# Optimization experiments

Hardware: AMD Instinct MI355X
Metric: run time of the kernel (lower is better)

Reference implementation:

```python
import jax, jax.numpy as jnp
import numpy as np

T, B, C = 2048, 8, 1024
H, K, P = 16, 31, 15  # num_heads, kernel_size, padding_l
R = C // H


def setup_inputs() -> dict:
    key = jax.random.key(0)
    k1, k2 = jax.random.split(key)
    x = jax.random.normal(k1, (T, B, C), dtype=jnp.float32)
    # weight_linear.weight, xavier-ish scale, shape (H*K, C)
    W = jax.random.normal(k2, (H * K, C), dtype=jnp.float32) * (2.0 / (C + H * K)) ** 0.5
    return {"x": x, "W": W}


def reference(x, W):
    # per-position dynamic kernels: (T,B,H,K)
    w = jnp.einsum('tbc,oc->tbo', x, W).reshape(T, B, H, K)
    w = jax.nn.softmax(w, axis=-1)  # weight_softmax=True
    # depthwise dynamic conv: out[t] = sum_k w[t,:,:,k] * x[t - P + k]
    xr = x.reshape(T, B, H, R)
    xp = jnp.pad(xr, ((P, K - 1 - P), (0, 0), (0, 0), (0, 0)))
    out = jnp.zeros_like(xr)
    for k in range(K):  # fixed small kernel-size loop, fuses under jit
        out = out + w[:, :, :, k:k + 1] * jax.lax.dynamic_slice_in_dim(xp, k, T, axis=0)
    return out.reshape(T, B, C)
```

## Files before the change

kernel.cpp:

```cpp
#include <hip/hip_runtime.h>
#include <cstddef>
#include <cstdint>

constexpr int T_ = 2048;
constexpr int B_ = 8;
constexpr int C_ = 1024;
constexpr int H_ = 16;
constexpr int K_ = 31;
constexpr int P_ = 15;
constexpr int M_ = T_ * B_;
constexpr int N_ = H_ * K_;
constexpr int NP = 512;

typedef _Float16 f16x4 __attribute__((ext_vector_type(4)));
typedef _Float16 f16x8 __attribute__((ext_vector_type(8)));
typedef float f32x4 __attribute__((ext_vector_type(4)));

__device__ __forceinline__ void async_cp16(const void* g, void* l) {
    __builtin_amdgcn_global_load_lds(
        (const __attribute__((address_space(1))) void*)g,
        (__attribute__((address_space(3))) void*)l, 16, 0, 0);
}

constexpr int XCH = M_ * C_ / 8;
constexpr int WCH = NP * C_ / 8;

__global__ __launch_bounds__(256)
void cvt_inputs(const float* __restrict__ X, const float* __restrict__ W,
                _Float16* __restrict__ Xh, _Float16* __restrict__ Wh) {
    const int id = blockIdx.x * 256 + threadIdx.x;
    if (id < XCH) {
        const float4 v0 = *(const float4*)(X + (size_t)id * 8);
        const float4 v1 = *(const float4*)(X + (size_t)id * 8 + 4);
        f16x8 hv;
        hv[0] = (_Float16)v0.x; hv[1] = (_Float16)v0.y;
        hv[2] = (_Float16)v0.z; hv[3] = (_Float16)v0.w;
        hv[4] = (_Float16)v1.x; hv[5] = (_Float16)v1.y;
        hv[6] = (_Float16)v1.z; hv[7] = (_Float16)v1.w;
        *(f16x8*)(Xh + (size_t)id * 8) = hv;
    } else {
        const int j = id - XCH;
        const int n = j >> 7, sp = j & 127;
        const int h = n >> 5, k = n & 31;
        f16x8 hv = {};
        if (k < 31) {
            const float* wp = W + (size_t)(h * 31 + k) * C_ + sp * 8;
            const float4 v0 = *(const float4*)(wp);
            const float4 v1 = *(const float4*)(wp + 4);
            hv[0] = (_Float16)v0.x; hv[1] = (_Float16)v0.y;
            hv[2] = (_Float16)v0.z; hv[3] = (_Float16)v0.w;
            hv[4] = (_Float16)v1.x; hv[5] = (_Float16)v1.y;
            hv[6] = (_Float16)v1.z; hv[7] = (_Float16)v1.w;
        }
        *(f16x8*)(Wh + (size_t)n * C_ + sp * 8) = hv;
    }
}

__global__ __launch_bounds__(256)
void fused_gsc(const _Float16* __restrict__ Xh, const _Float16* __restrict__ Wh,
               float* __restrict__ out) {
    __shared__ __align__(16) char smem[81920];
    _Float16* const As = (_Float16*)smem;
    _Float16* const Bs = (_Float16*)(smem + 49152);
    _Float16* const Ls = (_Float16*)smem;
    _Float16* const Wls = (_Float16*)(smem + 49152);
    float (* const xs)[64] = (float(*)[64])smem;

    const int tid = threadIdx.x;
    const int lane = tid & 63;
    const int w = tid >> 6;
    const int wm = (w >> 1) * 64;
    const int wn = (w & 1) * 64;
    const int col = lane & 15;
    const int g = lane >> 4;
    const int m0 = blockIdx.x * 128;
    const int n0 = blockIdx.y * 128;

    const _Float16* asrc[4];
    const _Float16* bsrc[4];
#pragma unroll
    for (int p = 0; p < 4; ++p) {
        const int ci = p * 256 + tid;
        const int r = ci >> 3, cs = ci & 7;
        const int cl = cs ^ (r & 7);
        asrc[p] = Xh + (size_t)(m0 + r) * C_ + cl * 8;
        bsrc[p] = Wh + (size_t)(n0 + r) * C_ + cl * 8;
    }

    f32x4 acc[4][4] = {};

#pragma unroll
    for (int p = 0; p < 4; ++p) {
        const int ci = p * 256 + tid;
        async_cp16(asrc[p], As + ci * 8);
    }
#pragma unroll
    for (int p = 0; p < 4; ++p) {
        const int ci = p * 256 + tid;
        async_cp16(bsrc[p], Bs + ci * 8);
    }
#pragma unroll
    for (int p = 0; p < 4; ++p) {
        const int ci = p * 256 + tid;
        async_cp16(asrc[p] + 64, As + 8192 + ci * 8);
    }
    asm volatile("s_waitcnt vmcnt(4)" ::: "memory");
    __builtin_amdgcn_s_barrier();
    __builtin_amdgcn_sched_barrier(0);

    for (int t = 0; t < 16; ++t) {
        const int ca = t % 3, cb = t & 1;
        if (t < 15) {
            const int k1 = (t + 1) * 64;
#pragma unroll
            for (int p = 0; p < 4; ++p) {
                const int ci = p * 256 + tid;
                async_cp16(bsrc[p] + k1, Bs + (cb ^ 1) * 8192 + ci * 8);
            }
        }
        if (t < 14) {
            const int k2 = (t + 2) * 64;
            const int ca2 = (t + 2) % 3;
#pragma unroll
            for (int p = 0; p < 4; ++p) {
                const int ci = p * 256 + tid;
                async_cp16(asrc[p] + k2, As + ca2 * 8192 + ci * 8);
            }
        }

        f16x8 a[2][4], b[2][4];
#pragma unroll
        for (int kk = 0; kk < 2; ++kk) {
#pragma unroll
            for (int mf = 0; mf < 4; ++mf) {
                const int row = wm + mf * 16 + col;
                const int c = ((kk << 2) | g) ^ (row & 7);
                a[kk][mf] = *(const f16x8*)&As[ca * 8192 + row * 64 + c * 8];
            }
#pragma unroll
            for (int nf = 0; nf < 4; ++nf) {
                const int row = wn + nf * 16 + col;
                const int c = ((kk << 2) | g) ^ (row & 7);
                b[kk][nf] = *(const f16x8*)&Bs[cb * 8192 + row * 64 + c * 8];
            }
        }
#pragma unroll
        for (int kk = 0; kk < 2; ++kk)
#pragma unroll
            for (int nf = 0; nf < 4; ++nf)
#pragma unroll
                for (int mf = 0; mf < 4; ++mf)
                    acc[mf][nf] = __builtin_amdgcn_mfma_f32_16x16x32_f16(
                        a[kk][mf], b[kk][nf], acc[mf][nf], 0, 0, 0);

        if (t < 14) {
            asm volatile("s_waitcnt vmcnt(4)" ::: "memory");
        } else {
            asm volatile("s_waitcnt vmcnt(0)" ::: "memory");
        }
        __builtin_amdgcn_s_barrier();
        __builtin_amdgcn_sched_barrier(0);
    }

    const int rb = g * 4;
#pragma unroll
    for (int nf = 0; nf < 4; ++nf) {
        const int nl = wn + nf * 16 + col;
#pragma unroll
        for (int mf = 0; mf < 4; ++mf) {
            const int row = wm + mf * 16 + rb;
#pragma unroll
            for (int r = 0; r < 4; ++r)
                Ls[(row + r) * 136 + nl] = (_Float16)acc[mf][nf][r];
        }
    }
    __syncthreads();

#pragma unroll
    for (int p = 0; p < 2; ++p) {
        const int task = tid + p * 256;
        const int row = task >> 2, hl = task & 3;
        const _Float16* lp = &Ls[row * 136 + hl * 32];
        float v[32];
#pragma unroll
        for (int c = 0; c < 4; ++c) {
            const f16x8 ch = *(const f16x8*)(lp + c * 8);
#pragma unroll
            for (int e = 0; e < 8; ++e) v[c * 8 + e] = (float)ch[e];
        }
        float mx = v[0];
#pragma unroll
        for (int k = 1; k < 31; ++k) mx = fmaxf(mx, v[k]);
        float ssum = 0.f;
#pragma unroll
        for (int k = 0; k < 31; ++k) { v[k] = __expf(v[k] - mx); ssum += v[k]; }
        const float inv = 1.f / ssum;
        _Float16* op = &Wls[(hl * 128 + row) * 32];
#pragma unroll
        for (int c = 0; c < 4; ++c) {
            f16x8 ov;
#pragma unroll
            for (int e = 0; e < 8; ++e) {
                const int k = c * 8 + e;
                ov[e] = (k < 31) ? (_Float16)(v[k] * inv) : (_Float16)0.f;
            }
            *(f16x8*)(op + c * 8) = ov;
        }
    }

    const int t0 = blockIdx.x * 16;
    const int hbase = blockIdx.y * 4;
    const int s = tid & 15;
    const int grp = tid >> 4;
    const int bl = grp & 3;
    const int tquad = (grp >> 2) * 4;

    for (int iter = 0; iter < 8; ++iter) {
        const int hl = iter >> 1, bh = iter & 1;
        const int h = hbase + hl;
        __syncthreads();

        for (int task = tid; task < 184 * 8; task += 256) {
            const int r184 = task >> 3, hc = task & 7;
            const int r46 = r184 >> 2, bb = r184 & 3;
            const int t = t0 + r46 - 15;
            f16x8 v = {};
            if (t >= 0 && t < T_)
                v = *(const f16x8*)(Xh + (size_t)(t * 8 + bh * 4 + bb) * C_ +
                                    h * 64 + hc * 8);
            f32x4 lo, hi;
            lo[0] = (float)v[0]; lo[1] = (float)v[1];
            lo[2] = (float)v[2]; lo[3] = (float)v[3];
            hi[0] = (float)v[4]; hi[1] = (float)v[5];
            hi[2] = (float)v[6]; hi[3] = (float)v[7];
            const int sw = r184 & 7;
            *(f32x4*)&xs[r184][((2 * hc) ^ sw) * 4] = lo;
            *(f32x4*)&xs[r184][((2 * hc + 1) ^ sw) * 4] = hi;
        }
        __syncthreads();

        const int bglob = bh * 4 + bl;
        f32x4 cacc[4] = {};
        f32x4 wc[4];
#pragma unroll
        for (int rr = 0; rr < 34; ++rr) {
            const int r184 = (tquad + rr) * 4 + bl;
            const f32x4 xv = *(const f32x4*)&xs[r184][(s ^ (r184 & 7)) * 4];
#pragma unroll
            for (int i = 0; i < 4; ++i) {
                const int k = rr - i;
                if (k < 0 || k > 30) continue;
                if ((k & 3) == 0) {
                    const f16x4 wq = *(const f16x4*)
                        &Wls[(hl * 128 + (tquad + i) * 8 + bglob) * 32 + k];
                    wc[i][0] = (float)wq[0]; wc[i][1] = (float)wq[1];
                    wc[i][2] = (float)wq[2]; wc[i][3] = (float)wq[3];
                }
                cacc[i] += wc[i][k & 3] * xv;
            }
        }
#pragma unroll
        for (int i = 0; i < 4; ++i) {
            const int t = t0 + tquad + i;
            *(f32x4*)(out + (size_t)(t * 8 + bglob) * C_ + h * 64 + s * 4) =
                cacc[i];
        }
    }
}

extern "C" void kernel_launch(void* const* d_in, const int* in_sizes, int n_in,
                              void* d_out, int out_size, void* d_ws,
                              size_t ws_size, hipStream_t stream) {
    const float* X = (const float*)d_in[0];
    const float* W = (const float*)d_in[1];
    float* out = (float*)d_out;

    _Float16* Wh = (_Float16*)d_ws;
    _Float16* Xh = (_Float16*)((char*)d_ws + (size_t)NP * C_ * 2);

    cvt_inputs<<<(XCH + WCH) / 256, 256, 0, stream>>>(X, W, Xh, Wh);
    fused_gsc<<<dim3(M_ / 128, NP / 128), 256, 0, stream>>>(Xh, Wh, out);
}
```

Measured before the change: 76.13 us.

## Retile fused GEMM+conv blocks to 64 timesteps by 2 batches for halo reuse

Measured after the change: 83.83 us. 1.1x slower.

```diff
diff --git a/kernel.cpp b/kernel.cpp
--- a/kernel.cpp
+++ b/kernel.cpp
@@ -73,8 +73,11 @@
     const int wn = (w & 1) * 64;
     const int col = lane & 15;
     const int g = lane >> 4;
-    const int m0 = blockIdx.x * 128;
-    const int n0 = blockIdx.y * 128;
+    const int bx = (int)blockIdx.x;
+    const int t0 = (bx >> 2) * 64;
+    const int b0 = (bx & 3) * 2;
+    const int n0 = (int)blockIdx.y * 128;
+    const int hbase = (int)blockIdx.y * 4;
 
     const _Float16* asrc[4];
     const _Float16* bsrc[4];
@@ -83,7 +86,8 @@
         const int ci = p * 256 + tid;
         const int r = ci >> 3, cs = ci & 7;
         const int cl = cs ^ (r & 7);
-        asrc[p] = Xh + (size_t)(m0 + r) * C_ + cl * 8;
+        const int m = (t0 + (r >> 1)) * 8 + b0 + (r & 1);
+        asrc[p] = Xh + (size_t)m * C_ + cl * 8;
         bsrc[p] = Wh + (size_t)(n0 + r) * C_ + cl * 8;
     }
 
@@ -208,62 +212,63 @@
         }
     }
 
-    const int t0 = blockIdx.x * 16;
-    const int hbase = blockIdx.y * 4;
     const int s = tid & 15;
     const int grp = tid >> 4;
-    const int bl = grp & 3;
-    const int tquad = (grp >> 2) * 4;
-
-    for (int iter = 0; iter < 8; ++iter) {
-        const int hl = iter >> 1, bh = iter & 1;
+    const int bl = grp & 1;
+    const int tqb = (grp >> 1) * 8;
+
+    for (int hl = 0; hl < 4; ++hl) {
         const int h = hbase + hl;
         __syncthreads();
 
-        for (int task = tid; task < 184 * 8; task += 256) {
-            const int r184 = task >> 3, hc = task & 7;
-            const int r46 = r184 >> 2, bb = r184 & 3;
-            const int t = t0 + r46 - 15;
+        for (int task = tid; task < 188 * 8; task += 256) {
+            const int r = task >> 3, hc = task & 7;
+            const int tp = t0 + (r >> 1) - 15;
+            const int bb = b0 + (r & 1);
             f16x8 v = {};
-            if (t >= 0 && t < T_)
-                v = *(const f16x8*)(Xh + (size_t)(t * 8 + bh * 4 + bb) * C_ +
+            if (tp >= 0 && tp < T_)
+                v = *(const f16x8*)(Xh + (size_t)(tp * 8 + bb) * C_ +
                                     h * 64 + hc * 8);
             f32x4 lo, hi;
             lo[0] = (float)v[0]; lo[1] = (float)v[1];
             lo[2] = (float)v[2]; lo[3] = (float)v[3];
             hi[0] = (float)v[4]; hi[1] = (float)v[5];
             hi[2] = (float)v[6]; hi[3] = (float)v[7];
-            const int sw = r184 & 7;
-            *(f32x4*)&xs[r184][((2 * hc) ^ sw) * 4] = lo;
-            *(f32x4*)&xs[r184][((2 * hc + 1) ^ sw) * 4] = hi;
+            const int sw = r & 7;
+            *(f32x4*)&xs[r][((2 * hc) ^ sw) * 4] = lo;
+            *(f32x4*)&xs[r][((2 * hc + 1) ^ sw) * 4] = hi;
         }
         __syncthreads();
 
-        const int bglob = bh * 4 + bl;
-        f32x4 cacc[4] = {};
-        f32x4 wc[4];
-#pragma unroll
-        for (int rr = 0; rr < 34; ++rr) {
-            const int r184 = (tquad + rr) * 4 + bl;
-            const f32x4 xv = *(const f32x4*)&xs[r184][(s ^ (r184 & 7)) * 4];
+#pragma unroll
+        for (int qq = 0; qq < 2; ++qq) {
+            const int tquad = tqb + qq * 4;
+            f32x4 cacc[4] = {};
+            f32x4 wc[4];
+#pragma unroll
+            for (int rr = 0; rr < 34; ++rr) {
+                const int r = (tquad + rr) * 2 + bl;
+                const f32x4 xv = *(const f32x4*)&xs[r][(s ^ (r & 7)) * 4];
+#pragma unroll
+                for (int i = 0; i < 4; ++i) {
+                    const int k = rr - i;
+                    if (k < 0 || k > 30) continue;
+                    if ((k & 3) == 0) {
+                        const int row = (tquad + i) * 2 + bl;
+                        const f16x4 wq = *(const f16x4*)
+                            &Wls[(hl * 128 + row) * 32 + k];
+                        wc[i][0] = (float)wq[0]; wc[i][1] = (float)wq[1];
+                        wc[i][2] = (float)wq[2]; wc[i][3] = (float)wq[3];
+                    }
+                    cacc[i] += wc[i][k & 3] * xv;
+                }
+            }
 #pragma unroll
             for (int i = 0; i < 4; ++i) {
-                const int k = rr - i;
-                if (k < 0 || k > 30) continue;
-                if ((k & 3) == 0) {
-                    const f16x4 wq = *(const f16x4*)
-                        &Wls[(hl * 128 + (tquad + i) * 8 + bglob) * 32 + k];
-                    wc[i][0] = (float)wq[0]; wc[i][1] = (float)wq[1];
-                    wc[i][2] = (float)wq[2]; wc[i][3] = (float)wq[3];
-                }
-                cacc[i] += wc[i][k & 3] * xv;
-            }
-        }
-#pragma unroll
-        for (int i = 0; i < 4; ++i) {
-            const int t = t0 + tquad + i;
-            *(f32x4*)(out + (size_t)(t * 8 + bglob) * C_ + h * 64 + s * 4) =
-                cacc[i];
+                const int t = t0 + tquad + i;
+                *(f32x4*)(out + (size_t)(t * 8 + b0 + bl) * C_ +
+                          h * 64 + s * 4) = cacc[i];
+            }
         }
     }
 }
@@ -279,5 +284,5 @@
     _Float16* Xh = (_Float16*)((char*)d_ws + (size_t)NP * C_ * 2);
 
     cvt_inputs<<<(XCH + WCH) / 256, 256, 0, stream>>>(X, W, Xh, Wh);
-    fused_gsc<<<dim3(M_ / 128, NP / 128), 256, 0, stream>>>(Xh, Wh, out);
-}
+    fused_gsc<<<dim3(128, 4), 256, 0, stream>>>(Xh, Wh, out);
+}
```
